# Performance work log

Measured on AMD Instinct MI355X. Metric: run time of the kernel, lower is better.

Reference implementation:

```python
import jax, jax.numpy as jnp
import numpy as np

PAD = 1  # padding from init_kwargs

def setup_inputs() -> dict:
    key = jax.random.key(0)
    k1, k2 = jax.random.split(key)
    x = jax.random.normal(k1, (1, 256, 224, 224), dtype=jnp.float32)
    # Conv2d_mvm weight: [out_channels, in_channels, kh, kw]
    weight = jax.random.normal(k2, (256, 256, 3, 3), dtype=jnp.float32) * 0.05
    return {"x": x, "weight": weight}

def reference(x, weight):
    # Exact math of the bit-sliced crossbar conv forward: stride-1 cross-correlation
    # with zero padding, no bias, output squeezed to [C_out, H_out, W_out]
    # (the original forward emits no batch dimension).
    out = jax.lax.conv_general_dilated(
        x, weight,
        window_strides=(1, 1),
        padding=((PAD, PAD), (PAD, PAD)),
        dimension_numbers=("NCHW", "OIHW", "NCHW"),
    )
    return out[0]  # [C_out, H_out, W_out]
```

## Files before the change

kernel.cpp:

```cpp
#include <hip/hip_runtime.h>


#define H 224
#define W 224
#define NPOS (H*W)
#define CI 256
#define CO 256
#define KDIM 2304
#define HP 226
#define XP_ELEMS (HP*HP*CI)
#define AP_ELEMS (CO*KDIM)

typedef __bf16 bf16x8 __attribute__((ext_vector_type(8)));
typedef float f32x4 __attribute__((ext_vector_type(4)));

__device__ __forceinline__ unsigned short f2bf(float f) {
    unsigned int u = __float_as_uint(f);
    u += 0x7fff + ((u >> 16) & 1);
    return (unsigned short)(u >> 16);
}

__device__ __forceinline__ void load_lds16(const unsigned short* g, unsigned short* l) {
    __builtin_amdgcn_global_load_lds(
        (const __attribute__((address_space(1))) void*)g,
        (__attribute__((address_space(3))) void*)l,
        16, 0, 0);
}

__global__ void prologue_kernel(const float* __restrict__ w, unsigned short* __restrict__ ap,
                                unsigned short* __restrict__ xp) {
    if (blockIdx.x < AP_ELEMS / 256) {
        int o = blockIdx.x * 256 + threadIdx.x;
        int co = o / KDIM;
        int rem = o - co * KDIM;
        int tap = rem >> 8;
        int ci = rem & 255;
        ap[o] = f2bf(w[(co * CI + ci) * 9 + tap]);
    } else {
        int idx = (blockIdx.x - AP_ELEMS / 256) * 256 + threadIdx.x;
        int hp, wp, ci;
        if (idx < 2 * HP * CI) {
            int r = idx / (HP * CI);
            int rem = idx - r * (HP * CI);
            hp = r * (HP - 1);
            wp = rem / CI;
            ci = rem & (CI - 1);
        } else {
            int i2 = idx - 2 * HP * CI;
            int side = i2 / (H * CI);
            int rem = i2 - side * (H * CI);
            hp = 1 + rem / CI;
            wp = side * (HP - 1);
            ci = rem & (CI - 1);
        }
        xp[(hp * HP + wp) * CI + ci] = 0;
    }
}

__global__ void xtrans_kernel(const float* __restrict__ x, unsigned short* __restrict__ xp) {
    __shared__ unsigned short tile[64][66];
    const unsigned int pBase = blockIdx.x * 64;
    const unsigned int ciBase = blockIdx.y * 64;
    const unsigned int t = threadIdx.x;
    {
        const unsigned int p_l = t & 63;
        const unsigned int c0 = t >> 6;
#pragma unroll
        for (int i = 0; i < 16; ++i) {
            const unsigned int ci_l = c0 + i * 4;
            tile[ci_l][p_l] = f2bf(x[(ciBase + ci_l) * NPOS + pBase + p_l]);
        }
    }
    __syncthreads();
    {
        const unsigned int ci_l = t & 63;
        const unsigned int p0 = t >> 6;
#pragma unroll
        for (int i = 0; i < 16; ++i) {
            const unsigned int p_l = p0 + i * 4;
            const unsigned int p = pBase + p_l;
            const unsigned int hi = p / W;
            const unsigned int wi = p - hi * W;
            xp[((hi + 1) * HP + (wi + 1)) * CI + ciBase + ci_l] = tile[ci_l][p_l];
        }
    }
}

__global__ __launch_bounds__(256, 3) void gemm_conv_kernel(
    const unsigned short* __restrict__ Ap,
    const unsigned short* __restrict__ Xp,
    float* __restrict__ out)
{
    __shared__ unsigned short Als[2][4096];
    __shared__ unsigned short Bls[2][4096];

    const int tid = threadIdx.x;
    const int Nb = blockIdx.x;
    const int Mb = blockIdx.y;
    const int wave = tid >> 6;
    const int wm = wave >> 1;
    const int wn = wave & 1;
    const int lane = tid & 63;
    const int ln15 = lane & 15;
    const int quad = lane >> 4;
    const int sw = ln15 & 3;

    const int l2 = lane >> 2;
    const int c4 = (lane & 3) ^ (l2 & 3);

    const unsigned short* a_src[2];
    const unsigned short* b_src[2];
#pragma unroll
    for (int j = 0; j < 2; ++j) {
        const int row = (wave * 2 + j) * 16 + l2;
        a_src[j] = Ap + (Mb * 128 + row) * KDIM + c4 * 8;
        unsigned int p = Nb * 128 + row;
        unsigned int hi = p / W, wi = p - hi * W;
        b_src[j] = Xp + (hi * HP + wi) * CI + c4 * 8;
    }

    f32x4 acc[4][4];
#pragma unroll
    for (int mi = 0; mi < 4; ++mi)
#pragma unroll
        for (int ni = 0; ni < 4; ++ni)
            acc[mi][ni] = (f32x4){0.f, 0.f, 0.f, 0.f};

    auto stage = [&](int kc, int buf) {
        const int tap = kc >> 3;
        const int dh = tap / 3, dw = tap - dh * 3;
        const int boff = (dh * HP + dw) * CI + (kc & 7) * 32;
        const int aoff = kc * 32;
#pragma unroll
        for (int j = 0; j < 2; ++j) {
            load_lds16(a_src[j] + aoff, &Als[buf][(wave * 2 + j) * 512]);
            load_lds16(b_src[j] + boff, &Bls[buf][(wave * 2 + j) * 512]);
        }
    };

    stage(0, 0);
    __syncthreads();

    for (int kc = 0; kc < 72; ++kc) {
        const int cur = kc & 1;
        if (kc < 71) stage(kc + 1, cur ^ 1);

        bf16x8 af[4], bfr[4];
#pragma unroll
        for (int mi = 0; mi < 4; ++mi)
            af[mi] = *(const bf16x8*)&Als[cur][(wm * 64 + mi * 16 + ln15) * 32 +
                                              ((quad ^ sw) * 8)];
#pragma unroll
        for (int ni = 0; ni < 4; ++ni)
            bfr[ni] = *(const bf16x8*)&Bls[cur][(wn * 64 + ni * 16 + ln15) * 32 +
                                               ((quad ^ sw) * 8)];
#pragma unroll
        for (int mi = 0; mi < 4; ++mi)
#pragma unroll
            for (int ni = 0; ni < 4; ++ni)
                acc[mi][ni] = __builtin_amdgcn_mfma_f32_16x16x32_bf16(
                    af[mi], bfr[ni], acc[mi][ni], 0, 0, 0);

        __syncthreads();
    }

    const int pcol = Nb * 128 + wn * 64 + ln15;
    const int corow = Mb * 128 + wm * 64 + quad * 4;
#pragma unroll
    for (int mi = 0; mi < 4; ++mi)
#pragma unroll
        for (int ni = 0; ni < 4; ++ni)
#pragma unroll
            for (int r = 0; r < 4; ++r)
                out[(corow + mi * 16 + r) * NPOS + pcol + ni * 16] = acc[mi][ni][r];
}

extern "C" void kernel_launch(void* const* d_in, const int* in_sizes, int n_in,
                              void* d_out, int out_size, void* d_ws, size_t ws_size,
                              hipStream_t stream) {
    const float* x = (const float*)d_in[0];
    const float* w = (const float*)d_in[1];
    float* out = (float*)d_out;

    unsigned short* xp = (unsigned short*)d_ws;
    unsigned short* ap = xp + XP_ELEMS;

    prologue_kernel<<<AP_ELEMS / 256 + 900, 256, 0, stream>>>(w, ap, xp);
    xtrans_kernel<<<dim3(NPOS / 64, CI / 64), 256, 0, stream>>>(x, xp);
    gemm_conv_kernel<<<dim3(NPOS / 128, CO / 128), 256, 0, stream>>>(ap, xp, out);
}
```

Measured before the change: 184.6 us.

## Merge prologue and transpose kernels into one vectorized prep kernel

```diff
diff --git a/kernel.cpp b/kernel.cpp
--- a/kernel.cpp
+++ b/kernel.cpp
@@ -13,6 +13,9 @@
 
 typedef __bf16 bf16x8 __attribute__((ext_vector_type(8)));
 typedef float f32x4 __attribute__((ext_vector_type(4)));
+typedef unsigned short u16x4 __attribute__((ext_vector_type(4)));
+typedef unsigned short u16x8 __attribute__((ext_vector_type(8)));
+typedef float f32x4v __attribute__((ext_vector_type(4)));
 
 __device__ __forceinline__ unsigned short f2bf(float f) {
     unsigned int u = __float_as_uint(f);
@@ -27,61 +30,74 @@
         16, 0, 0);
 }
 
-__global__ void prologue_kernel(const float* __restrict__ w, unsigned short* __restrict__ ap,
-                                unsigned short* __restrict__ xp) {
-    if (blockIdx.x < AP_ELEMS / 256) {
-        int o = blockIdx.x * 256 + threadIdx.x;
-        int co = o / KDIM;
-        int rem = o - co * KDIM;
-        int tap = rem >> 8;
-        int ci = rem & 255;
-        ap[o] = f2bf(w[(co * CI + ci) * 9 + tap]);
+#define XT_BLOCKS 3136
+#define WT_BLOCKS 256
+#define BORDER_V8 28800
+#define ROW_V8 7232
+__global__ void prep_kernel(const float* __restrict__ x, const float* __restrict__ w,
+                            unsigned short* __restrict__ ap, unsigned short* __restrict__ xp) {
+    __shared__ unsigned short smem[64 * 68];
+    const int bx = blockIdx.x;
+    const int t = threadIdx.x;
+
+    if (bx < XT_BLOCKS) {
+        const unsigned int pBase = (unsigned int)(bx % 784) * 64;
+        const unsigned int ciBase = (unsigned int)(bx / 784) * 64;
+        {
+            const int p4 = (t & 15) * 4;
+            const int c0 = t >> 4;
+#pragma unroll
+            for (int i = 0; i < 4; ++i) {
+                const int ci_l = c0 + i * 16;
+                const f32x4 v = *(const f32x4*)&x[(ciBase + ci_l) * NPOS + pBase + p4];
+                u16x4 s;
+                s[0] = f2bf(v[0]); s[1] = f2bf(v[1]); s[2] = f2bf(v[2]); s[3] = f2bf(v[3]);
+                *(u16x4*)&smem[ci_l * 68 + p4] = s;
+            }
+        }
+        __syncthreads();
+        {
+            const int ci0 = (t & 7) * 8;
+            const int pr = t >> 3;
+#pragma unroll
+            for (int j = 0; j < 2; ++j) {
+                const int p_l = pr + j * 32;
+                const unsigned int p = pBase + p_l;
+                const unsigned int hi = p / W, wi = p - hi * W;
+                u16x8 v;
+#pragma unroll
+                for (int k = 0; k < 8; ++k) v[k] = smem[(ci0 + k) * 68 + p_l];
+                *(u16x8*)&xp[((hi + 1) * HP + (wi + 1)) * CI + ciBase + ci0] = v;
+            }
+        }
+    } else if (bx < XT_BLOCKS + WT_BLOCKS) {
+        const int co = bx - XT_BLOCKS;
+        const float* wc = w + co * KDIM;
+#pragma unroll
+        for (int i = 0; i < 9; ++i)
+            smem[i * 256 + t] = f2bf(wc[i * 256 + t]);
+        __syncthreads();
+        unsigned short* apc = ap + co * KDIM;
+#pragma unroll
+        for (int tap = 0; tap < 9; ++tap)
+            apc[tap * 256 + t] = smem[t * 9 + tap];
     } else {
-        int idx = (blockIdx.x - AP_ELEMS / 256) * 256 + threadIdx.x;
-        int hp, wp, ci;
-        if (idx < 2 * HP * CI) {
-            int r = idx / (HP * CI);
-            int rem = idx - r * (HP * CI);
-            hp = r * (HP - 1);
-            wp = rem / CI;
-            ci = rem & (CI - 1);
-        } else {
-            int i2 = idx - 2 * HP * CI;
-            int side = i2 / (H * CI);
-            int rem = i2 - side * (H * CI);
-            hp = 1 + rem / CI;
-            wp = side * (HP - 1);
-            ci = rem & (CI - 1);
-        }
-        xp[(hp * HP + wp) * CI + ci] = 0;
-    }
-}
-
-__global__ void xtrans_kernel(const float* __restrict__ x, unsigned short* __restrict__ xp) {
-    __shared__ unsigned short tile[64][66];
-    const unsigned int pBase = blockIdx.x * 64;
-    const unsigned int ciBase = blockIdx.y * 64;
-    const unsigned int t = threadIdx.x;
-    {
-        const unsigned int p_l = t & 63;
-        const unsigned int c0 = t >> 6;
-#pragma unroll
-        for (int i = 0; i < 16; ++i) {
-            const unsigned int ci_l = c0 + i * 4;
-            tile[ci_l][p_l] = f2bf(x[(ciBase + ci_l) * NPOS + pBase + p_l]);
-        }
-    }
-    __syncthreads();
-    {
-        const unsigned int ci_l = t & 63;
-        const unsigned int p0 = t >> 6;
-#pragma unroll
-        for (int i = 0; i < 16; ++i) {
-            const unsigned int p_l = p0 + i * 4;
-            const unsigned int p = pBase + p_l;
-            const unsigned int hi = p / W;
-            const unsigned int wi = p - hi * W;
-            xp[((hi + 1) * HP + (wi + 1)) * CI + ciBase + ci_l] = tile[ci_l][p_l];
+        const int idx = (bx - XT_BLOCKS - WT_BLOCKS) * 256 + t;
+        if (idx < BORDER_V8) {
+            unsigned short* p;
+            if (idx < 2 * ROW_V8) {
+                const int r = idx / ROW_V8;
+                const int off = idx - r * ROW_V8;
+                p = xp + r * (225 * HP * CI) + off * 8;
+            } else {
+                const int i2 = idx - 2 * ROW_V8;
+                const int seg = i2 >> 5;
+                const int o = i2 & 31;
+                const int hp = 1 + (seg >> 1);
+                const int wp = (seg & 1) * 225;
+                p = xp + (hp * HP + wp) * CI + o * 8;
+            }
+            *(u16x8*)p = (u16x8){0, 0, 0, 0, 0, 0, 0, 0};
         }
     }
 }
@@ -185,7 +201,6 @@
     unsigned short* xp = (unsigned short*)d_ws;
     unsigned short* ap = xp + XP_ELEMS;
 
-    prologue_kernel<<<AP_ELEMS / 256 + 900, 256, 0, stream>>>(w, ap, xp);
-    xtrans_kernel<<<dim3(NPOS / 64, CI / 64), 256, 0, stream>>>(x, xp);
+    prep_kernel<<<XT_BLOCKS + WT_BLOCKS + 113, 256, 0, stream>>>(x, w, ap, xp);
     gemm_conv_kernel<<<dim3(NPOS / 128, CO / 128), 256, 0, stream>>>(ap, xp, out);
 }
```

New measurement: 180.6 us. 2.2% less time.
